# Kernel tuning notes

Hardware: AMD Instinct MI355X
Metric: run time of the kernel (lower is better)

## Reference

```python
import jax, jax.numpy as jnp
import numpy as np

N = 50000      # nodes
E = 800000     # directed edges (avg degree 16)
F_IN = 128     # dataset.num_features
H = 256        # hidden_channels
C = 40         # dataset.num_classes


def _glorot(k, shape):
    lim = float(np.sqrt(6.0 / (shape[0] + shape[1])))
    return jax.random.uniform(k, shape, jnp.float32, -lim, lim)


def setup_inputs() -> dict:
    key = jax.random.key(0)
    ks = jax.random.split(key, 8)
    x = jax.random.normal(ks[0], (N, F_IN), jnp.float32)
    edge_index = jax.random.randint(ks[1], (2, E), 0, N, dtype=jnp.int32)
    W1 = _glorot(ks[2], (F_IN, H));      b1 = jnp.zeros((H,), jnp.float32)
    W2 = _glorot(ks[3], (H, H // 2));    b2 = jnp.zeros((H // 2,), jnp.float32)
    W3 = _glorot(ks[4], (H // 2, H // 4)); b3 = jnp.zeros((H // 4,), jnp.float32)
    W4 = _glorot(ks[5], (H // 4, C));    b4 = jnp.zeros((C,), jnp.float32)
    return {"x": x, "edge_index": edge_index,
            "W1": W1, "b1": b1, "W2": W2, "b2": b2,
            "W3": W3, "b3": b3, "W4": W4, "b4": b4}


def reference(x, edge_index, W1, b1, W2, b2, W3, b3, W4, b4):
    # GCNConv with default add_self_loops=True and symmetric normalization.
    loops = jnp.arange(N, dtype=edge_index.dtype)
    src = jnp.concatenate([edge_index[0], loops])   # message sources
    dst = jnp.concatenate([edge_index[1], loops])   # aggregation targets
    # degree computed on target index (PyG default), incl. self-loops
    deg = jax.ops.segment_sum(jnp.ones_like(dst, jnp.float32), dst, num_segments=N)
    dinv = jnp.where(deg > 0, jax.lax.rsqrt(deg), 0.0)
    norm = dinv[src] * dinv[dst]                    # [E+N]

    def conv(h, W, b):
        h = h @ W                                   # transform first (PyG order)
        msg = h[src] * norm[:, None]                # gather + scale
        return jax.ops.segment_sum(msg, dst, num_segments=N) + b

    h = jax.nn.relu(conv(x, W1, b1))   # dropout = identity in eval mode
    h = jax.nn.relu(conv(h, W2, b2))
    h = jax.nn.relu(conv(h, W3, b3))
    return conv(h, W4, b4)
```

## Files before the change

### kernel.cpp

```cpp
#include <hip/hip_runtime.h>
#include <stdint.h>

#define NNODES 50000
#define NEDGES 800000
#define NB ((NNODES + 255) / 256)
#define EPB 4096
#define SCAT_NBLK ((NEDGES + EPB - 1) / EPB)

typedef __attribute__((ext_vector_type(8))) short bf16x8;
typedef __attribute__((ext_vector_type(4))) float f32x4;

__device__ inline unsigned short f2bf(float f) {
    unsigned u = __float_as_uint(f);
    return (unsigned short)((u + 0x7fffu + ((u >> 16) & 1u)) >> 16);
}
__device__ inline float bf2f(unsigned short h) {
    return __uint_as_float(((unsigned)h) << 16);
}


__global__ void zero_kernel(int* __restrict__ p, int n) {
    int i = blockIdx.x * blockDim.x + threadIdx.x;
    if (i < n) p[i] = 0;
}

__global__ __launch_bounds__(256) void bucket_count_kernel(const int* __restrict__ dst,
                                                           int* __restrict__ bhist) {
    __shared__ int h[NB];
    for (int b = threadIdx.x; b < NB; b += 256) h[b] = 0;
    __syncthreads();
    const int base = blockIdx.x * EPB;
#pragma unroll
    for (int i = 0; i < EPB / 256; ++i) {
        const int e = base + threadIdx.x + i * 256;
        if (e < NEDGES) atomicAdd(&h[dst[e] >> 8], 1);
    }
    __syncthreads();
    for (int b = threadIdx.x; b < NB; b += 256)
        if (h[b]) atomicAdd(&bhist[b], h[b]);
}

__global__ __launch_bounds__(256) void bucket_scan_kernel(const int* __restrict__ bhist,
                                                          int* __restrict__ bofs,
                                                          int* __restrict__ gcur,
                                                          int* __restrict__ rp_last) {
    __shared__ int s[256];
    const int t = threadIdx.x;
    s[t] = (t < NB) ? bhist[t] : 0;
    __syncthreads();
    for (int off = 1; off < 256; off <<= 1) {
        int v = (t >= off) ? s[t - off] : 0;
        __syncthreads();
        s[t] += v;
        __syncthreads();
    }
    if (t < NB) {
        const int excl = (t > 0) ? s[t - 1] : 0;
        bofs[t] = excl;
        gcur[t] = excl;
    }
    if (t == 255) { bofs[NB] = s[255]; rp_last[0] = s[255]; }
}

__global__ __launch_bounds__(256) void bucket_scatter_kernel(const int* __restrict__ src,
                                                             const int* __restrict__ dst,
                                                             int* __restrict__ gcur,
                                                             unsigned* __restrict__ gpk) {
    __shared__ int h[256];
    __shared__ int s[256];
    __shared__ int gof[256];
    __shared__ unsigned pr[EPB];
    __shared__ int ga[EPB];

    const int t = threadIdx.x;
    const int base = blockIdx.x * EPB;
    const int nval = min(EPB, NEDGES - base);

    h[t] = 0;
    __syncthreads();
#pragma unroll
    for (int i = 0; i < EPB / 256; ++i) {
        const int e = base + t + i * 256;
        if (e < NEDGES) atomicAdd(&h[dst[e] >> 8], 1);
    }
    __syncthreads();
    s[t] = h[t];
    __syncthreads();
    for (int off = 1; off < 256; off <<= 1) {
        int v = (t >= off) ? s[t - off] : 0;
        __syncthreads();
        s[t] += v;
        __syncthreads();
    }
    {
        const int c = h[t];
        if (t < NB && c > 0) gof[t] = atomicAdd(&gcur[t], c);
        const int lofs = s[t] - c;
        h[t] = lofs;
        s[t] = lofs;
    }
    __syncthreads();
#pragma unroll
    for (int i = 0; i < EPB / 256; ++i) {
        const int e = base + t + i * 256;
        if (e < NEDGES) {
            const int d = dst[e];
            const int b = d >> 8;
            const int slot = atomicAdd(&h[b], 1);
            pr[slot] = ((unsigned)(d & 255) << 16) | (unsigned)src[e];
            ga[slot] = gof[b] + (slot - s[b]);
        }
    }
    __syncthreads();
#pragma unroll
    for (int i = 0; i < EPB / 256; ++i) {
        const int slot = t + i * 256;
        if (slot < nval) gpk[ga[slot]] = pr[slot];
    }
}

__global__ __launch_bounds__(256) void csr_fill_kernel(const unsigned* __restrict__ gpk,
                                                       const int* __restrict__ bofs,
                                                       int* __restrict__ rp,
                                                       float* __restrict__ dinv,
                                                       int* __restrict__ col) {
    __shared__ int c[256];
    __shared__ int s[256];
    __shared__ int cur[256];
    const int t = threadIdx.x;
    const int b = blockIdx.x;
    const int beg = bofs[b], end = bofs[b + 1];
    c[t] = 0;
    __syncthreads();
    for (int e = beg + t; e < end; e += 256) atomicAdd(&c[gpk[e] >> 16], 1);
    __syncthreads();
    s[t] = c[t];
    __syncthreads();
    for (int off = 1; off < 256; off <<= 1) {
        int v = (t >= off) ? s[t - off] : 0;
        __syncthreads();
        s[t] += v;
        __syncthreads();
    }
    const int excl = s[t] - c[t];
    cur[t] = excl;
    const int node = b * 256 + t;
    if (node < NNODES) {
        rp[node] = beg + excl;
        dinv[node] = rsqrtf((float)(c[t] + 1));
    }
    __syncthreads();
    for (int e = beg + t; e < end; e += 256) {
        const unsigned p = gpk[e];
        const int r = atomicAdd(&cur[p >> 16], 1);
        col[beg + r] = (int)(p & 0xffffu);
    }
}


__global__ __launch_bounds__(256) void cvt_kernel(const float* __restrict__ in,
                                                  unsigned short* __restrict__ out, int n4) {
    int i = blockIdx.x * 256 + threadIdx.x;
    if (i >= n4) return;
    float4 v = *(const float4*)(in + (size_t)i * 4);
    ushort4 h;
    h.x = f2bf(v.x); h.y = f2bf(v.y); h.z = f2bf(v.z); h.w = f2bf(v.w);
    *(ushort4*)(out + (size_t)i * 4) = h;
}


template <int VEC>
__device__ inline void vloadf(float (&d)[VEC], const float* __restrict__ p) {
    if constexpr (VEC == 2) { float2 t = *(const float2*)p; d[0]=t.x; d[1]=t.y; }
    else { d[0] = *p; }
}
template <int VEC>
__device__ inline void vloadbf(float (&d)[VEC], const unsigned short* __restrict__ p) {
    if constexpr (VEC == 2) {
        unsigned v = *(const unsigned*)p;
        d[0] = bf2f((unsigned short)(v & 0xffffu));
        d[1] = bf2f((unsigned short)(v >> 16));
    } else {
        d[0] = bf2f(*p);
    }
}
template <int VEC>
__device__ inline void vstoref(float* __restrict__ p, const float (&d)[VEC]) {
    if constexpr (VEC == 2) { *(float2*)p = make_float2(d[0], d[1]); }
    else { *p = d[0]; }
}

template <int F, int VEC, bool RELU, bool HAS_BIAS>
__global__ __launch_bounds__(256) void agg_kernel(const float* __restrict__ in32,
                                                  const unsigned short* __restrict__ inbf,
                                                  float* __restrict__ out,
                                                  const int* __restrict__ rp,
                                                  const int* __restrict__ colidx,
                                                  const float* __restrict__ dinv,
                                                  const float* __restrict__ bias) {
    const int wave = threadIdx.x >> 6;
    const int lane = threadIdx.x & 63;
    const int d = blockIdx.x * 4 + wave;
    if (d >= NNODES) return;
    constexpr int LANES = F / VEC;
    if (lane >= LANES) return;
    const int off = lane * VEC;

    const float dv = dinv[d];
    float acc[VEC];
    vloadf<VEC>(acc, in32 + (size_t)d * F + off);
#pragma unroll
    for (int v = 0; v < VEC; ++v) acc[v] *= dv;

    int j = rp[d];
    const int end = rp[d + 1];
    for (; j + 4 <= end; j += 4) {
        const int c0 = colidx[j + 0], c1 = colidx[j + 1], c2 = colidx[j + 2], c3 = colidx[j + 3];
        const float w0 = dinv[c0], w1 = dinv[c1], w2 = dinv[c2], w3 = dinv[c3];
        float t0[VEC], t1[VEC], t2[VEC], t3[VEC];
        vloadbf<VEC>(t0, inbf + (size_t)c0 * F + off);
        vloadbf<VEC>(t1, inbf + (size_t)c1 * F + off);
        vloadbf<VEC>(t2, inbf + (size_t)c2 * F + off);
        vloadbf<VEC>(t3, inbf + (size_t)c3 * F + off);
#pragma unroll
        for (int v = 0; v < VEC; ++v) acc[v] += w0 * t0[v] + w1 * t1[v] + w2 * t2[v] + w3 * t3[v];
    }
    for (; j < end; ++j) {
        const int c = colidx[j];
        const float wc = dinv[c];
        float t[VEC];
        vloadbf<VEC>(t, inbf + (size_t)c * F + off);
#pragma unroll
        for (int v = 0; v < VEC; ++v) acc[v] += wc * t[v];
    }

    float res[VEC];
#pragma unroll
    for (int v = 0; v < VEC; ++v) {
        float r = dv * acc[v];
        if constexpr (HAS_BIAS) r += bias[off + v];
        if constexpr (RELU) r = fmaxf(r, 0.0f);
        res[v] = r;
    }
    vstoref<VEC>(out + (size_t)d * F + off, res);
}


template <int K, int M>
__global__ __launch_bounds__(256) void repack_kernel(const float* __restrict__ W,
                                                     unsigned short* __restrict__ hi,
                                                     unsigned short* __restrict__ lo) {
    int i = blockIdx.x * 256 + threadIdx.x;
    if (i >= K * M) return;
    const int k = i / M, n = i % M;
    constexpr int KS = K / 32;
    const int cb = n >> 7;
    const int ct = (n >> 4) & 7;
    const int ln = ((k >> 3) & 3) * 16 + (n & 15);
    const int j  = k & 7;
    const int ks = k >> 5;
    const size_t o = ((((size_t)cb * KS + ks) * 8 + ct) * 64 + ln) * 8 + j;
    const float f = W[i];
    const unsigned short h = f2bf(f);
    hi[o] = h;
    lo[o] = f2bf(f - bf2f(h));
}


template <int K, int M, int BM, bool BIAS_RELU, bool WRITE_BF>
__global__ __launch_bounds__(256) void mfma_gemm_kernel(const float* __restrict__ A,
                                                        const unsigned short* __restrict__ Whi,
                                                        const unsigned short* __restrict__ Wlo,
                                                        const float* __restrict__ bias,
                                                        float* __restrict__ C,
                                                        unsigned short* __restrict__ Cbf) {
    constexpr int KS = K / 32;
    constexpr int ASZ = BM * 64;
    constexpr int CI = (BM == 128) ? 4 : 2;
    __shared__ char lds[2 * ASZ + 16384];
    char* Ahi = lds;
    char* Alo = lds + ASZ;
    char* Bhi = lds + 2 * ASZ;
    char* Blo = lds + 2 * ASZ + 8192;

    const int t = threadIdx.x;
    const int lane = t & 63;
    const int w = t >> 6;
    const int wr = (BM == 128) ? (w >> 1) : 0;
    const int wc = (BM == 128) ? (w & 1) : w;
    const int r0 = blockIdx.x * BM;
    const int n0 = blockIdx.y * 128;

    const unsigned short* bhg = Whi + (size_t)blockIdx.y * KS * 4096;
    const unsigned short* blg = Wlo + (size_t)blockIdx.y * KS * 4096;

    f32x4 acc[4][CI];
#pragma unroll
    for (int i = 0; i < 4; ++i)
#pragma unroll
        for (int j = 0; j < CI; ++j) acc[i][j] = (f32x4){0.f, 0.f, 0.f, 0.f};

    for (int ks = 0; ks < KS; ++ks) {
        const int k0 = ks * 32;

        {
            const char* gh = (const char*)(bhg + (size_t)ks * 4096);
            const char* gl = (const char*)(blg + (size_t)ks * 4096);
#pragma unroll
            for (int c = 0; c < 2; ++c) {
                const int ct = w * 2 + c;
                __builtin_amdgcn_global_load_lds(
                    (const __attribute__((address_space(1))) void*)(gh + ct * 1024 + lane * 16),
                    (__attribute__((address_space(3))) void*)(Bhi + ct * 1024), 16, 0, 0);
                __builtin_amdgcn_global_load_lds(
                    (const __attribute__((address_space(1))) void*)(gl + ct * 1024 + lane * 16),
                    (__attribute__((address_space(3))) void*)(Blo + ct * 1024), 16, 0, 0);
            }
        }

        float4 av[BM / 32];
#pragma unroll
        for (int i = 0; i < BM / 32; ++i) {
            const int q = t + i * 256;
            const int row = q >> 3;
            const int kq = (q & 7) * 4;
            const int gr = r0 + row;
            float4 v = make_float4(0.f, 0.f, 0.f, 0.f);
            if (gr < NNODES) v = *(const float4*)(A + (size_t)gr * K + k0 + kq);
            av[i] = v;
        }
#pragma unroll
        for (int i = 0; i < BM / 32; ++i) {
            const int q = t + i * 256;
            const int row = q >> 3;
            const int kq = (q & 7) * 4;
            const int rt = row >> 4, m = row & 15, quad = kq >> 3, j0 = kq & 7;
            const int off = rt * 1024 + (quad * 16 + m) * 16 + j0 * 2;
            const float4 v = av[i];
            ushort4 h, l;
            h.x = f2bf(v.x); l.x = f2bf(v.x - bf2f(h.x));
            h.y = f2bf(v.y); l.y = f2bf(v.y - bf2f(h.y));
            h.z = f2bf(v.z); l.z = f2bf(v.z - bf2f(h.z));
            h.w = f2bf(v.w); l.w = f2bf(v.w - bf2f(h.w));
            *(ushort4*)(Ahi + off) = h;
            *(ushort4*)(Alo + off) = l;
        }
        __syncthreads();

        bf16x8 ah[4], al[4], bh[CI], bl[CI];
#pragma unroll
        for (int i = 0; i < 4; ++i) {
            ah[i] = *(const bf16x8*)(Ahi + (wr * 4 + i) * 1024 + lane * 16);
            al[i] = *(const bf16x8*)(Alo + (wr * 4 + i) * 1024 + lane * 16);
        }
#pragma unroll
        for (int j = 0; j < CI; ++j) {
            bh[j] = *(const bf16x8*)(Bhi + (wc * CI + j) * 1024 + lane * 16);
            bl[j] = *(const bf16x8*)(Blo + (wc * CI + j) * 1024 + lane * 16);
        }
#pragma unroll
        for (int i = 0; i < 4; ++i)
#pragma unroll
            for (int j = 0; j < CI; ++j) {
                acc[i][j] = __builtin_amdgcn_mfma_f32_16x16x32_bf16(ah[i], bh[j], acc[i][j], 0, 0, 0);
                acc[i][j] = __builtin_amdgcn_mfma_f32_16x16x32_bf16(ah[i], bl[j], acc[i][j], 0, 0, 0);
                acc[i][j] = __builtin_amdgcn_mfma_f32_16x16x32_bf16(al[i], bh[j], acc[i][j], 0, 0, 0);
            }
        __syncthreads();
    }

    const int quad = lane >> 4;
    const int cl = lane & 15;
#pragma unroll
    for (int i = 0; i < 4; ++i) {
#pragma unroll
        for (int j = 0; j < CI; ++j) {
            const int colg = n0 + wc * (CI * 16) + j * 16 + cl;
            float bv = 0.f;
            if constexpr (BIAS_RELU) bv = bias[colg];
#pragma unroll
            for (int r = 0; r < 4; ++r) {
                const int rowg = r0 + wr * 64 + i * 16 + quad * 4 + r;
                if (rowg < NNODES) {
                    float v = acc[i][j][r] + bv;
                    if constexpr (BIAS_RELU) v = fmaxf(v, 0.f);
                    C[(size_t)rowg * M + colg] = v;
                    if constexpr (WRITE_BF) Cbf[(size_t)rowg * M + colg] = f2bf(v);
                }
            }
        }
    }
}


template <int BM, int BN, int BK, int TM, int TN, bool BIAS_RELU, bool WRITE_BF>
__global__ __launch_bounds__(256) void gemm_kernel(const float* __restrict__ A,
                                                   const float* __restrict__ W,
                                                   const float* __restrict__ bias,
                                                   float* __restrict__ C,
                                                   unsigned short* __restrict__ Cbf,
                                                   int Nrows, int K, int M) {
    constexpr int TX = BN / TN;
    constexpr int TY = BM / TM;
    static_assert(TX * TY == 256, "thread grid must be 256");
    constexpr int A_LOADS = (BM * BK) / (256 * 4);
    constexpr int W_LOADS = (BN * BK) / (256 * 4);
    static_assert(A_LOADS >= 1 && W_LOADS >= 1, "tile too small");

    const int tid = threadIdx.x;
    const int tx = tid % TX;
    const int ty = tid / TX;
    const int r0 = blockIdx.x * BM;
    const int c0 = blockIdx.y * BN;

    __shared__ float As[BK][BM + 4];
    __shared__ float Ws[BK][BN];

    float acc[TM][TN] = {};

    for (int k0 = 0; k0 < K; k0 += BK) {
#pragma unroll
        for (int l = 0; l < A_LOADS; ++l) {
            const int idx = tid + l * 256;
            const int row = idx / (BK / 4);
            const int kq = idx % (BK / 4);
            float4 v = make_float4(0.f, 0.f, 0.f, 0.f);
            const int gr = r0 + row;
            if (gr < Nrows) v = *(const float4*)(A + (size_t)gr * K + k0 + kq * 4);
            As[kq * 4 + 0][row] = v.x;
            As[kq * 4 + 1][row] = v.y;
            As[kq * 4 + 2][row] = v.z;
            As[kq * 4 + 3][row] = v.w;
        }
#pragma unroll
        for (int l = 0; l < W_LOADS; ++l) {
            const int idx = tid + l * 256;
            const int kk = idx / (BN / 4);
            const int cq = idx % (BN / 4);
            const int gc = c0 + cq * 4;
            float4 v;
            const float* wrow = W + (size_t)(k0 + kk) * M;
            if (gc + 3 < M) {
                v = *(const float4*)(wrow + gc);
            } else {
                v.x = (gc + 0 < M) ? wrow[gc + 0] : 0.f;
                v.y = (gc + 1 < M) ? wrow[gc + 1] : 0.f;
                v.z = (gc + 2 < M) ? wrow[gc + 2] : 0.f;
                v.w = (gc + 3 < M) ? wrow[gc + 3] : 0.f;
            }
            *(float4*)&Ws[kk][cq * 4] = v;
        }
        __syncthreads();

#pragma unroll
        for (int kk = 0; kk < BK; ++kk) {
            float a[TM], b[TN];
#pragma unroll
            for (int i = 0; i < TM; ++i) a[i] = As[kk][ty * TM + i];
#pragma unroll
            for (int j = 0; j < TN; ++j) b[j] = Ws[kk][tx * TN + j];
#pragma unroll
            for (int i = 0; i < TM; ++i)
#pragma unroll
                for (int j = 0; j < TN; ++j) acc[i][j] += a[i] * b[j];
        }
        __syncthreads();
    }

#pragma unroll
    for (int i = 0; i < TM; ++i) {
        const int gr = r0 + ty * TM + i;
        if (gr >= Nrows) continue;
#pragma unroll
        for (int j = 0; j < TN; ++j) {
            const int gc = c0 + tx * TN + j;
            if (gc >= M) continue;
            float v = acc[i][j];
            if constexpr (BIAS_RELU) v = fmaxf(v + bias[gc], 0.0f);
            C[(size_t)gr * M + gc] = v;
            if constexpr (WRITE_BF) Cbf[(size_t)gr * M + gc] = f2bf(v);
        }
    }
}


extern "C" void kernel_launch(void* const* d_in, const int* in_sizes, int n_in,
                              void* d_out, int out_size, void* d_ws, size_t ws_size,
                              hipStream_t stream) {
    const float* x  = (const float*)d_in[0];
    const int* ei   = (const int*)d_in[1];
    const float* W1 = (const float*)d_in[2];
    const float* b1 = (const float*)d_in[3];
    const float* W2 = (const float*)d_in[4];
    const float* b2 = (const float*)d_in[5];
    const float* W3 = (const float*)d_in[6];
    const float* b3 = (const float*)d_in[7];
    const float* W4 = (const float*)d_in[8];
    const float* b4 = (const float*)d_in[9];
    float* out = (float*)d_out;
    const int* esrc = ei;
    const int* edst = ei + NEDGES;

    char* w = (char*)d_ws;
    auto alloc = [&](size_t bytes) -> void* {
        void* p = (void*)w;
        w += (bytes + 255) & ~(size_t)255;
        return p;
    };
    int* rp     = (int*)alloc((size_t)(NNODES + 1) * 4);
    int* col    = (int*)alloc((size_t)NEDGES * 4);
    float* dinv = (float*)alloc((size_t)NNODES * 4);
    int* bhist  = (int*)alloc((size_t)NB * 4);
    int* bofs   = (int*)alloc((size_t)(NB + 1) * 4);
    int* gcur   = (int*)alloc((size_t)NB * 4);
    unsigned* gpk = (unsigned*)alloc((size_t)NEDGES * 4);
    unsigned short* W1hi = (unsigned short*)alloc((size_t)128 * 256 * 2);
    unsigned short* W1lo = (unsigned short*)alloc((size_t)128 * 256 * 2);
    unsigned short* W2hi = (unsigned short*)alloc((size_t)256 * 128 * 2);
    unsigned short* W2lo = (unsigned short*)alloc((size_t)256 * 128 * 2);
    float* B0   = (float*)alloc((size_t)NNODES * 256 * 4);
    float* B1   = (float*)alloc((size_t)NNODES * 128 * 4);
    float* B2   = (float*)alloc((size_t)NNODES * 128 * 4);
    unsigned short* xbf  = (unsigned short*)alloc((size_t)NNODES * 128 * 2);
    unsigned short* B1bf = (unsigned short*)alloc((size_t)NNODES * 128 * 2);
    unsigned short* B0bf = (unsigned short*)alloc((size_t)NNODES * 64 * 2);

    repack_kernel<128, 256><<<(128 * 256 + 255) / 256, 256, 0, stream>>>(W1, W1hi, W1lo);
    repack_kernel<256, 128><<<(256 * 128 + 255) / 256, 256, 0, stream>>>(W2, W2hi, W2lo);
    cvt_kernel<<<(NNODES * 128 / 4 + 255) / 256, 256, 0, stream>>>(x, xbf, NNODES * 128 / 4);

    zero_kernel<<<1, 256, 0, stream>>>(bhist, NB);
    bucket_count_kernel<<<SCAT_NBLK, 256, 0, stream>>>(edst, bhist);
    bucket_scan_kernel<<<1, 256, 0, stream>>>(bhist, bofs, gcur, rp + NNODES);
    bucket_scatter_kernel<<<SCAT_NBLK, 256, 0, stream>>>(esrc, edst, gcur, gpk);
    csr_fill_kernel<<<NB, 256, 0, stream>>>(gpk, bofs, rp, dinv, col);

    const int aggGrid = (NNODES + 3) / 4;
    const int rowBlks64 = (NNODES + 63) / 64;

    agg_kernel<128, 2, false, false><<<aggGrid, 256, 0, stream>>>(x, xbf, B2, rp, col, dinv, nullptr);
    mfma_gemm_kernel<128, 256, 64, true, false>
        <<<dim3(rowBlks64, 2), 256, 0, stream>>>(B2, W1hi, W1lo, b1, B0, nullptr);

    mfma_gemm_kernel<256, 128, 64, false, true>
        <<<dim3(rowBlks64, 1), 256, 0, stream>>>(B0, W2hi, W2lo, nullptr, B1, B1bf);
    agg_kernel<128, 2, true, true><<<aggGrid, 256, 0, stream>>>(B1, B1bf, B2, rp, col, dinv, b2);

    gemm_kernel<64, 64, 16, 4, 4, false, true>
        <<<dim3(rowBlks64, 1), 256, 0, stream>>>(B2, W3, nullptr, B0, B0bf, NNODES, 128, 64);
    agg_kernel<64, 1, true, true><<<aggGrid, 256, 0, stream>>>(B0, B0bf, B1, rp, col, dinv, b3);

    gemm_kernel<64, 64, 16, 4, 4, false, true>
        <<<dim3(rowBlks64, 1), 256, 0, stream>>>(B1, W4, nullptr, B0, B0bf, NNODES, 64, 40);
    agg_kernel<40, 1, false, true><<<aggGrid, 256, 0, stream>>>(B0, B0bf, out, rp, col, dinv, b4);
}
```

Baseline: 365.9 us.

## Prescale bf16 features by source dinv, shrink col to u16, split-edge aggregation

Result: no change. 369.6 us (+1.0%).

```diff
diff --git a/kernel.cpp b/kernel.cpp
--- a/kernel.cpp
+++ b/kernel.cpp
@@ -123,7 +123,7 @@
                                                        const int* __restrict__ bofs,
                                                        int* __restrict__ rp,
                                                        float* __restrict__ dinv,
-                                                       int* __restrict__ col) {
+                                                       unsigned short* __restrict__ col) {
     __shared__ int c[256];
     __shared__ int s[256];
     __shared__ int cur[256];
@@ -153,96 +153,163 @@
     for (int e = beg + t; e < end; e += 256) {
         const unsigned p = gpk[e];
         const int r = atomicAdd(&cur[p >> 16], 1);
-        col[beg + r] = (int)(p & 0xffffu);
+        col[beg + r] = (unsigned short)(p & 0xffffu);
     }
 }
 
 
 __global__ __launch_bounds__(256) void cvt_kernel(const float* __restrict__ in,
+                                                  const float* __restrict__ dinv,
                                                   unsigned short* __restrict__ out, int n4) {
     int i = blockIdx.x * 256 + threadIdx.x;
     if (i >= n4) return;
+    const float dv = dinv[i >> 5];
     float4 v = *(const float4*)(in + (size_t)i * 4);
     ushort4 h;
-    h.x = f2bf(v.x); h.y = f2bf(v.y); h.z = f2bf(v.z); h.w = f2bf(v.w);
+    h.x = f2bf(dv * v.x); h.y = f2bf(dv * v.y); h.z = f2bf(dv * v.z); h.w = f2bf(dv * v.w);
     *(ushort4*)(out + (size_t)i * 4) = h;
 }
 
 
-template <int VEC>
-__device__ inline void vloadf(float (&d)[VEC], const float* __restrict__ p) {
-    if constexpr (VEC == 2) { float2 t = *(const float2*)p; d[0]=t.x; d[1]=t.y; }
-    else { d[0] = *p; }
-}
-template <int VEC>
-__device__ inline void vloadbf(float (&d)[VEC], const unsigned short* __restrict__ p) {
-    if constexpr (VEC == 2) {
-        unsigned v = *(const unsigned*)p;
-        d[0] = bf2f((unsigned short)(v & 0xffffu));
-        d[1] = bf2f((unsigned short)(v >> 16));
-    } else {
-        d[0] = bf2f(*p);
-    }
-}
-template <int VEC>
-__device__ inline void vstoref(float* __restrict__ p, const float (&d)[VEC]) {
-    if constexpr (VEC == 2) { *(float2*)p = make_float2(d[0], d[1]); }
-    else { *p = d[0]; }
-}
-
-template <int F, int VEC, bool RELU, bool HAS_BIAS>
-__global__ __launch_bounds__(256) void agg_kernel(const float* __restrict__ in32,
-                                                  const unsigned short* __restrict__ inbf,
-                                                  float* __restrict__ out,
-                                                  const int* __restrict__ rp,
-                                                  const int* __restrict__ colidx,
-                                                  const float* __restrict__ dinv,
-                                                  const float* __restrict__ bias) {
+template <bool RELU, bool HAS_BIAS>
+__global__ __launch_bounds__(256) void agg128_kernel(const float* __restrict__ in32,
+                                                     const unsigned short* __restrict__ inbf,
+                                                     float* __restrict__ out,
+                                                     const int* __restrict__ rp,
+                                                     const unsigned short* __restrict__ col,
+                                                     const float* __restrict__ dinv,
+                                                     const float* __restrict__ bias) {
     const int wave = threadIdx.x >> 6;
     const int lane = threadIdx.x & 63;
     const int d = blockIdx.x * 4 + wave;
     if (d >= NNODES) return;
-    constexpr int LANES = F / VEC;
-    if (lane >= LANES) return;
-    const int off = lane * VEC;
-
+    const int half = lane >> 5;
+    const int fl = lane & 31;
     const float dv = dinv[d];
-    float acc[VEC];
-    vloadf<VEC>(acc, in32 + (size_t)d * F + off);
-#pragma unroll
-    for (int v = 0; v < VEC; ++v) acc[v] *= dv;
-
+
+    float acc[4] = {0.f, 0.f, 0.f, 0.f};
+    if (half == 0) {
+        float4 s = *(const float4*)(in32 + (size_t)d * 128 + fl * 4);
+        acc[0] = dv * s.x; acc[1] = dv * s.y; acc[2] = dv * s.z; acc[3] = dv * s.w;
+    }
+
+    int j = rp[d] + half;
+    const int end = rp[d + 1];
+    for (; j + 2 < end; j += 4) {
+        const int c0 = col[j], c1 = col[j + 2];
+        ushort4 a0 = *(const ushort4*)(inbf + (size_t)c0 * 128 + fl * 4);
+        ushort4 a1 = *(const ushort4*)(inbf + (size_t)c1 * 128 + fl * 4);
+        acc[0] += bf2f(a0.x) + bf2f(a1.x);
+        acc[1] += bf2f(a0.y) + bf2f(a1.y);
+        acc[2] += bf2f(a0.z) + bf2f(a1.z);
+        acc[3] += bf2f(a0.w) + bf2f(a1.w);
+    }
+    if (j < end) {
+        const int c0 = col[j];
+        ushort4 a0 = *(const ushort4*)(inbf + (size_t)c0 * 128 + fl * 4);
+        acc[0] += bf2f(a0.x); acc[1] += bf2f(a0.y); acc[2] += bf2f(a0.z); acc[3] += bf2f(a0.w);
+    }
+
+#pragma unroll
+    for (int v = 0; v < 4; ++v) acc[v] += __shfl_down(acc[v], 32);
+
+    if (half == 0) {
+        float4 r;
+        float* pr = &r.x;
+#pragma unroll
+        for (int v = 0; v < 4; ++v) {
+            float t = dv * acc[v];
+            if constexpr (HAS_BIAS) t += bias[fl * 4 + v];
+            if constexpr (RELU) t = fmaxf(t, 0.0f);
+            pr[v] = t;
+        }
+        *(float4*)(out + (size_t)d * 128 + fl * 4) = r;
+    }
+}
+
+template <bool RELU, bool HAS_BIAS>
+__global__ __launch_bounds__(256) void agg64_kernel(const float* __restrict__ in32,
+                                                    const unsigned short* __restrict__ inbf,
+                                                    float* __restrict__ out,
+                                                    const int* __restrict__ rp,
+                                                    const unsigned short* __restrict__ col,
+                                                    const float* __restrict__ dinv,
+                                                    const float* __restrict__ bias) {
+    const int wave = threadIdx.x >> 6;
+    const int lane = threadIdx.x & 63;
+    const int d = blockIdx.x * 4 + wave;
+    if (d >= NNODES) return;
+    const int quarter = lane >> 4;
+    const int fl = lane & 15;
+    const float dv = dinv[d];
+
+    float acc[4] = {0.f, 0.f, 0.f, 0.f};
+    if (quarter == 0) {
+        float4 s = *(const float4*)(in32 + (size_t)d * 64 + fl * 4);
+        acc[0] = dv * s.x; acc[1] = dv * s.y; acc[2] = dv * s.z; acc[3] = dv * s.w;
+    }
+
+    int j = rp[d] + quarter;
+    const int end = rp[d + 1];
+    for (; j + 4 < end; j += 8) {
+        const int c0 = col[j], c1 = col[j + 4];
+        ushort4 a0 = *(const ushort4*)(inbf + (size_t)c0 * 64 + fl * 4);
+        ushort4 a1 = *(const ushort4*)(inbf + (size_t)c1 * 64 + fl * 4);
+        acc[0] += bf2f(a0.x) + bf2f(a1.x);
+        acc[1] += bf2f(a0.y) + bf2f(a1.y);
+        acc[2] += bf2f(a0.z) + bf2f(a1.z);
+        acc[3] += bf2f(a0.w) + bf2f(a1.w);
+    }
+    if (j < end) {
+        const int c0 = col[j];
+        ushort4 a0 = *(const ushort4*)(inbf + (size_t)c0 * 64 + fl * 4);
+        acc[0] += bf2f(a0.x); acc[1] += bf2f(a0.y); acc[2] += bf2f(a0.z); acc[3] += bf2f(a0.w);
+    }
+
+#pragma unroll
+    for (int v = 0; v < 4; ++v) {
+        acc[v] += __shfl_down(acc[v], 32);
+        acc[v] += __shfl_down(acc[v], 16);
+    }
+
+    if (quarter == 0) {
+        float4 r;
+        float* pr = &r.x;
+#pragma unroll
+        for (int v = 0; v < 4; ++v) {
+            float t = dv * acc[v];
+            if constexpr (HAS_BIAS) t += bias[fl * 4 + v];
+            if constexpr (RELU) t = fmaxf(t, 0.0f);
+            pr[v] = t;
+        }
+        *(float4*)(out + (size_t)d * 64 + fl * 4) = r;
+    }
+}
+
+__global__ __launch_bounds__(256) void agg40_kernel(const float* __restrict__ in32,
+                                                    const unsigned short* __restrict__ inbf,
+                                                    float* __restrict__ out,
+                                                    const int* __restrict__ rp,
+                                                    const unsigned short* __restrict__ col,
+                                                    const float* __restrict__ dinv,
+                                                    const float* __restrict__ bias) {
+    const int wave = threadIdx.x >> 6;
+    const int lane = threadIdx.x & 63;
+    const int d = blockIdx.x * 4 + wave;
+    if (d >= NNODES) return;
+    if (lane >= 40) return;
+    const float dv = dinv[d];
+
+    float acc = dv * in32[(size_t)d * 40 + lane];
     int j = rp[d];
     const int end = rp[d + 1];
-    for (; j + 4 <= end; j += 4) {
-        const int c0 = colidx[j + 0], c1 = colidx[j + 1], c2 = colidx[j + 2], c3 = colidx[j + 3];
-        const float w0 = dinv[c0], w1 = dinv[c1], w2 = dinv[c2], w3 = dinv[c3];
-        float t0[VEC], t1[VEC], t2[VEC], t3[VEC];
-        vloadbf<VEC>(t0, inbf + (size_t)c0 * F + off);
-        vloadbf<VEC>(t1, inbf + (size_t)c1 * F + off);
-        vloadbf<VEC>(t2, inbf + (size_t)c2 * F + off);
-        vloadbf<VEC>(t3, inbf + (size_t)c3 * F + off);
-#pragma unroll
-        for (int v = 0; v < VEC; ++v) acc[v] += w0 * t0[v] + w1 * t1[v] + w2 * t2[v] + w3 * t3[v];
-    }
-    for (; j < end; ++j) {
-        const int c = colidx[j];
-        const float wc = dinv[c];
-        float t[VEC];
-        vloadbf<VEC>(t, inbf + (size_t)c * F + off);
-#pragma unroll
-        for (int v = 0; v < VEC; ++v) acc[v] += wc * t[v];
-    }
-
-    float res[VEC];
-#pragma unroll
-    for (int v = 0; v < VEC; ++v) {
-        float r = dv * acc[v];
-        if constexpr (HAS_BIAS) r += bias[off + v];
-        if constexpr (RELU) r = fmaxf(r, 0.0f);
-        res[v] = r;
-    }
-    vstoref<VEC>(out + (size_t)d * F + off, res);
+    for (; j + 2 <= end; j += 2) {
+        const int c0 = col[j], c1 = col[j + 1];
+        acc += bf2f(inbf[(size_t)c0 * 40 + lane]) + bf2f(inbf[(size_t)c1 * 40 + lane]);
+    }
+    if (j < end) acc += bf2f(inbf[(size_t)col[j] * 40 + lane]);
+
+    out[(size_t)d * 40 + lane] = dv * acc + bias[lane];
 }
 
 
@@ -273,7 +340,8 @@
                                                         const unsigned short* __restrict__ Wlo,
                                                         const float* __restrict__ bias,
                                                         float* __restrict__ C,
-                                                        unsigned short* __restrict__ Cbf) {
+                                                        unsigned short* __restrict__ Cbf,
+                                                        const float* __restrict__ dinv) {
     constexpr int KS = K / 32;
     constexpr int ASZ = BM * 64;
     constexpr int CI = (BM == 128) ? 4 : 2;
@@ -385,7 +453,7 @@
                     float v = acc[i][j][r] + bv;
                     if constexpr (BIAS_RELU) v = fmaxf(v, 0.f);
                     C[(size_t)rowg * M + colg] = v;
-                    if constexpr (WRITE_BF) Cbf[(size_t)rowg * M + colg] = f2bf(v);
+                    if constexpr (WRITE_BF) Cbf[(size_t)rowg * M + colg] = f2bf(dinv[rowg] * v);
                 }
             }
         }
@@ -399,6 +467,7 @@
                                                    const float* __restrict__ bias,
                                                    float* __restrict__ C,
                                                    unsigned short* __restrict__ Cbf,
+                                                   const float* __restrict__ dinv,
                                                    int Nrows, int K, int M) {
     constexpr int TX = BN / TN;
     constexpr int TY = BM / TM;
@@ -471,6 +540,7 @@
     for (int i = 0; i < TM; ++i) {
         const int gr = r0 + ty * TM + i;
         if (gr >= Nrows) continue;
+        const float dvr = WRITE_BF ? dinv[gr] : 0.f;
 #pragma unroll
         for (int j = 0; j < TN; ++j) {
             const int gc = c0 + tx * TN + j;
@@ -478,7 +548,7 @@
             float v = acc[i][j];
             if constexpr (BIAS_RELU) v = fmaxf(v + bias[gc], 0.0f);
             C[(size_t)gr * M + gc] = v;
-            if constexpr (WRITE_BF) Cbf[(size_t)gr * M + gc] = f2bf(v);
+            if constexpr (WRITE_BF) Cbf[(size_t)gr * M + gc] = f2bf(dvr * v);
         }
     }
 }
@@ -508,7 +578,7 @@
         return p;
     };
     int* rp     = (int*)alloc((size_t)(NNODES + 1) * 4);
-    int* col    = (int*)alloc((size_t)NEDGES * 4);
+    unsigned short* col = (unsigned short*)alloc((size_t)NEDGES * 2);
     float* dinv = (float*)alloc((size_t)NNODES * 4);
     int* bhist  = (int*)alloc((size_t)NB * 4);
     int* bofs   = (int*)alloc((size_t)(NB + 1) * 4);
@@ -527,7 +597,6 @@
 
     repack_kernel<128, 256><<<(128 * 256 + 255) / 256, 256, 0, stream>>>(W1, W1hi, W1lo);
     repack_kernel<256, 128><<<(256 * 128 + 255) / 256, 256, 0, stream>>>(W2, W2hi, W2lo);
-    cvt_kernel<<<(NNODES * 128 / 4 + 255) / 256, 256, 0, stream>>>(x, xbf, NNODES * 128 / 4);
 
     zero_kernel<<<1, 256, 0, stream>>>(bhist, NB);
     bucket_count_kernel<<<SCAT_NBLK, 256, 0, stream>>>(edst, bhist);
@@ -535,22 +604,24 @@
     bucket_scatter_kernel<<<SCAT_NBLK, 256, 0, stream>>>(esrc, edst, gcur, gpk);
     csr_fill_kernel<<<NB, 256, 0, stream>>>(gpk, bofs, rp, dinv, col);
 
+    cvt_kernel<<<(NNODES * 128 / 4 + 255) / 256, 256, 0, stream>>>(x, dinv, xbf, NNODES * 128 / 4);
+
     const int aggGrid = (NNODES + 3) / 4;
     const int rowBlks64 = (NNODES + 63) / 64;
 
-    agg_kernel<128, 2, false, false><<<aggGrid, 256, 0, stream>>>(x, xbf, B2, rp, col, dinv, nullptr);
+    agg128_kernel<false, false><<<aggGrid, 256, 0, stream>>>(x, xbf, B2, rp, col, dinv, nullptr);
     mfma_gemm_kernel<128, 256, 64, true, false>
-        <<<dim3(rowBlks64, 2), 256, 0, stream>>>(B2, W1hi, W1lo, b1, B0, nullptr);
+        <<<dim3(rowBlks64, 2), 256, 0, stream>>>(B2, W1hi, W1lo, b1, B0, nullptr, nullptr);
 
     mfma_gemm_kernel<256, 128, 64, false, true>
-        <<<dim3(rowBlks64, 1), 256, 0, stream>>>(B0, W2hi, W2lo, nullptr, B1, B1bf);
-    agg_kernel<128, 2, true, true><<<aggGrid, 256, 0, stream>>>(B1, B1bf, B2, rp, col, dinv, b2);
+        <<<dim3(rowBlks64, 1), 256, 0, stream>>>(B0, W2hi, W2lo, nullptr, B1, B1bf, dinv);
+    agg128_kernel<true, true><<<aggGrid, 256, 0, stream>>>(B1, B1bf, B2, rp, col, dinv, b2);
 
     gemm_kernel<64, 64, 16, 4, 4, false, true>
-        <<<dim3(rowBlks64, 1), 256, 0, stream>>>(B2, W3, nullptr, B0, B0bf, NNODES, 128, 64);
-    agg_kernel<64, 1, true, true><<<aggGrid, 256, 0, stream>>>(B0, B0bf, B1, rp, col, dinv, b3);
+        <<<dim3(rowBlks64, 1), 256, 0, stream>>>(B2, W3, nullptr, B0, B0bf, dinv, NNODES, 128, 64);
+    agg64_kernel<true, true><<<aggGrid, 256, 0, stream>>>(B0, B0bf, B1, rp, col, dinv, b3);
 
     gemm_kernel<64, 64, 16, 4, 4, false, true>
-        <<<dim3(rowBlks64, 1), 256, 0, stream>>>(B1, W4, nullptr, B0, B0bf, NNODES, 64, 40);
-    agg_kernel<40, 1, false, true><<<aggGrid, 256, 0, stream>>>(B0, B0bf, out, rp, col, dinv, b4);
-}
+        <<<dim3(rowBlks64, 1), 256, 0, stream>>>(B1, W4, nullptr, B0, B0bf, dinv, NNODES, 64, 40);
+    agg40_kernel<<<aggGrid, 256, 0, stream>>>(B0, B0bf, out, rp, col, dinv, b4);
+}
```
